# Performance work log

Measured on AMD Instinct MI355X. Metric: run time of the kernel, lower is better.

## Reference

```python
import jax, jax.numpy as jnp
import numpy as np
import math

B, H, N, D = 2, 16, 8192, 64
NUM_PROJS = 7
BLOCK = 256   # key block size
SAMPLE = 256  # number of sampled columns


def _gray_perm(n):
    # AngularLSH._unit_hamming_distance_array: Gray-code ordering of 2**n buckets
    a = np.array([0, 1], dtype=np.int32)
    for i in range(1, n):
        a = np.concatenate([a, a[::-1] + 2 ** i])
    return a

PERM = jnp.asarray(_gray_perm(NUM_PROJS))
ENC = jnp.asarray(2 ** np.arange(NUM_PROJS), dtype=jnp.int32)


def lsh_hash(x, proj_dir):
    # sign-bit angular LSH, then Gray-code remap so nearby buckets share bits
    bits = (jnp.einsum('bhnd,dr->bhnr', x, proj_dir) > 0).astype(jnp.int32)
    bin_ids = (bits * ENC).sum(-1)
    return PERM[bin_ids]


def take_seq(x, idx):
    # gather along the sequence axis (axis=2); idx is [B,H,M]
    return jnp.take_along_axis(x, idx[..., None], axis=2)


def setup_inputs() -> dict:
    key = jax.random.key(0)
    ks = jax.random.split(key, 5)
    return {
        'query': jax.random.normal(ks[0], (B, H, N, D), jnp.float32),
        'key': jax.random.normal(ks[1], (B, H, N, D), jnp.float32),
        'value': jax.random.normal(ks[2], (B, H, N, D), jnp.float32),
        'proj_dir': jax.random.normal(ks[3], (D + 1, NUM_PROJS), jnp.float32),
        'sampled_set': jax.random.randint(ks[4], (B, H, SAMPLE), 0, N),
    }


def reference(query, key, value, proj_dir, sampled_set):
    scale = D ** -0.5

    # asymmetric MIPS transform: key gets sqrt(max||k||^2 - ||k||^2), query gets 0
    k_norm = jnp.linalg.norm(key, axis=-1)                 # [B,H,N]
    k_max = jnp.max(k_norm, axis=-1, keepdims=True)        # [B,H,1]
    k_extra = jnp.sqrt(jnp.maximum(k_max ** 2 - k_norm ** 2, 0.0))
    key_aug = jnp.concatenate([key, k_extra[..., None]], axis=-1)
    query_aug = jnp.concatenate([query, jnp.zeros_like(query[..., :1])], axis=-1)

    # stable sort by LSH bucket; inverse permutation to un-sort queries at the end
    q_idx = jnp.argsort(lsh_hash(query_aug, proj_dir), axis=2, stable=True)
    k_idx = jnp.argsort(lsh_hash(key_aug, proj_dir), axis=2, stable=True)
    q_idx_inv = jnp.argsort(q_idx, axis=2, stable=True)

    q_s = take_seq(query, q_idx)
    k_s = take_seq(key, k_idx)
    v_s = take_seq(value, k_idx)

    nb = N // BLOCK      # number of key blocks (N divisible by BLOCK here)
    qbs = N // nb        # query block size

    # 1) block-diagonal exact attention over LSH-sorted blocks
    qb = q_s.reshape(B, H, nb, qbs, D)
    kb = k_s.reshape(B, H, nb, BLOCK, D)
    vb = v_s.reshape(B, H, nb, BLOCK, D)
    s_blk = jnp.einsum('bhgqd,bhgkd->bhgqk', qb, kb) * scale
    lse_blk = jax.nn.logsumexp(s_blk, axis=-1)             # [B,H,nb,qbs]
    attn_blk = jnp.einsum('bhgqk,bhgkd->bhgqd', jax.nn.softmax(s_blk, axis=-1), vb)
    attn_blk = attn_blk.reshape(B, H, N, D)
    lse_blk = lse_blk.reshape(B, H, N, 1)

    # 2) residual via uniformly sampled columns; mask out columns already in the
    #    query's own diagonal block to avoid double counting
    k_sub = take_seq(k_s, sampled_set)                     # [B,H,S,D]
    v_sub = take_seq(v_s, sampled_set)
    q_blk_id = jnp.arange(N) // qbs                        # [N]
    covered = q_blk_id[None, None, :, None] == (sampled_set // BLOCK)[:, :, None, :]
    bias = jnp.where(covered, jnp.finfo(q_s.dtype).min, 0.0)
    s_res = jnp.einsum('bhnd,bhsd->bhns', q_s, k_sub) * scale + bias
    # importance weight n_key/sample_size applied in log-space (approximate_unsampled)
    lse_res = jax.nn.logsumexp(s_res, axis=-1, keepdims=True) + math.log(N / SAMPLE)
    attn_res = jnp.einsum('bhns,bhsd->bhnd', jax.nn.softmax(s_res, axis=-1), v_sub)

    # add_self_attentions: merge the two softmax estimates in log-space
    c = 1.0 / (1.0 + jnp.exp(lse_res - lse_blk))
    attn = c * attn_blk + (1.0 - c) * attn_res

    # un-sort rows back to the original query order
    attn = take_seq(attn, q_idx_inv)
    return attn
```

## Files before the change

### kernel.cpp

```cpp
#include <hip/hip_runtime.h>
#include <hip/hip_bf16.h>
#include <math.h>

#define BD 2
#define HD 16
#define NSEQ 8192
#define DDIM 64
#define NPROJ 7
#define KBLK 256
#define NSAMP 256
#define NBH (BD*HD)
#define NB (NSEQ/KBLK)

#define LOG2E_8 0.18033688011112042f

typedef short bf16x8 __attribute__((ext_vector_type(8)));
typedef float f32x4 __attribute__((ext_vector_type(4)));

__device__ __forceinline__ unsigned int pk2bf(float a, float b) {
    union { __hip_bfloat162 h; unsigned int u; } t;
    t.h = __float22bfloat162_rn(make_float2(a, b));
    return t.u;
}

__global__ __launch_bounds__(256) void prelude_kernel(const float* __restrict__ q,
                                                      const float* __restrict__ k,
                                                      const float* __restrict__ pd,
                                                      float* __restrict__ kdots,
                                                      unsigned int* __restrict__ kmax_bits,
                                                      unsigned char* __restrict__ qh) {
    __shared__ float pds[(DDIM+1)*NPROJ];
    __shared__ float red[256];
    const int tid = threadIdx.x;
    for (int i = tid; i < (DDIM+1)*NPROJ; i += 256) pds[i] = pd[i];
    __syncthreads();

    const int lin = blockIdx.x * 256 + tid;
    const int bh = lin >> 13;

    float acc[NPROJ];
    float4 xv[16];

    {
        const float4* xp = (const float4*)(q + (size_t)lin * DDIM);
        #pragma unroll
        for (int j = 0; j < 16; ++j) xv[j] = xp[j];
        #pragma unroll
        for (int r = 0; r < NPROJ; ++r) acc[r] = 0.f;
        #pragma unroll
        for (int j = 0; j < 16; ++j) {
            float xs[4] = {xv[j].x, xv[j].y, xv[j].z, xv[j].w};
            #pragma unroll
            for (int c = 0; c < 4; ++c) {
                const int d = j*4 + c;
                #pragma unroll
                for (int r = 0; r < NPROJ; ++r) acc[r] += xs[c] * pds[d*NPROJ + r];
            }
        }
        int bin = 0;
        #pragma unroll
        for (int r = 0; r < NPROJ; ++r) bin |= (acc[r] > 0.f) << r;
        qh[lin] = (unsigned char)(bin ^ (bin >> 1));
    }

    float nr;
    {
        const float4* xp = (const float4*)(k + (size_t)lin * DDIM);
        #pragma unroll
        for (int j = 0; j < 16; ++j) xv[j] = xp[j];
        #pragma unroll
        for (int r = 0; r < NPROJ; ++r) acc[r] = 0.f;
        #pragma unroll
        for (int j = 0; j < 16; ++j) {
            float xs[4] = {xv[j].x, xv[j].y, xv[j].z, xv[j].w};
            #pragma unroll
            for (int c = 0; c < 4; ++c) {
                const int d = j*4 + c;
                #pragma unroll
                for (int r = 0; r < NPROJ; ++r) acc[r] += xs[c] * pds[d*NPROJ + r];
            }
        }
        float ss = 0.f;
        #pragma unroll
        for (int j = 0; j < 16; ++j) {
            float4 t = xv[j];
            ss += t.x*t.x + t.y*t.y + t.z*t.z + t.w*t.w;
        }
        nr = sqrtf(ss);
        float4* kd = (float4*)(kdots + (size_t)lin * 8);
        kd[0] = make_float4(acc[0], acc[1], acc[2], acc[3]);
        kd[1] = make_float4(acc[4], acc[5], acc[6], nr);
    }

    red[tid] = nr;
    __syncthreads();
    for (int s = 128; s > 0; s >>= 1) {
        if (tid < s) red[tid] = fmaxf(red[tid], red[tid+s]);
        __syncthreads();
    }
    if (tid == 0) atomicMax(&kmax_bits[bh], __float_as_uint(red[0]));
}

__global__ __launch_bounds__(256) void khash_kernel(const float* __restrict__ pd,
                                                    const float* __restrict__ kdots,
                                                    const unsigned int* __restrict__ kmax_bits,
                                                    unsigned char* __restrict__ kh) {
    const int lin = blockIdx.x * 256 + threadIdx.x;
    const int bh = lin >> 13;
    const float4* kd = (const float4*)(kdots + (size_t)lin * 8);
    float4 d0 = kd[0], d1 = kd[1];
    float acc[NPROJ] = {d0.x, d0.y, d0.z, d0.w, d1.x, d1.y, d1.z};
    const float kn = d1.w;
    const float km = __uint_as_float(kmax_bits[bh]);
    const float ex = sqrtf(fmaxf(km*km - kn*kn, 0.f));
    int bin = 0;
    #pragma unroll
    for (int r = 0; r < NPROJ; ++r) {
        acc[r] += ex * pd[DDIM*NPROJ + r];
        bin |= (acc[r] > 0.f) << r;
    }
    kh[lin] = (unsigned char)(bin ^ (bin >> 1));
}

__global__ __launch_bounds__(256) void sort_kernel(const unsigned char* __restrict__ qhash,
                                                   const unsigned char* __restrict__ khash,
                                                   int* __restrict__ qidx,
                                                   int* __restrict__ kidx) {
    __shared__ unsigned char hsh[NSEQ];
    __shared__ unsigned short cnt[128][264];
    __shared__ int base[128];
    __shared__ int wtot[2];
    const int bh = blockIdx.x, tid = threadIdx.x;
    const unsigned char* hash = blockIdx.y ? khash : qhash;
    int* idx = blockIdx.y ? kidx : qidx;

    {
        const uint4* src = (const uint4*)(hash + (size_t)bh * NSEQ);
        uint4* hdst = (uint4*)hsh;
        hdst[tid] = src[tid];
        hdst[tid + 256] = src[tid + 256];
        unsigned int* cz = (unsigned int*)&cnt[0][0];
        for (int i = tid; i < 128*264/2; i += 256) cz[i] = 0;
    }
    __syncthreads();
    {
        const unsigned char* s = hsh + tid*32;
        for (int i = 0; i < 32; ++i) cnt[s[i]][tid]++;
    }
    __syncthreads();

    int sc = 0, vv = 0;
    if (tid < 128) {
        unsigned run = 0;
        uint4* rp = (uint4*)cnt[tid];
        for (int wd = 0; wd < 32; ++wd) {
            uint4 x = rp[wd];
            unsigned v0 = x.x & 0xffffu, v1 = x.x >> 16;
            unsigned v2 = x.y & 0xffffu, v3 = x.y >> 16;
            unsigned v4 = x.z & 0xffffu, v5 = x.z >> 16;
            unsigned v6 = x.w & 0xffffu, v7 = x.w >> 16;
            unsigned p0 = run, p1 = p0+v0, p2 = p1+v1, p3 = p2+v2,
                     p4 = p3+v3, p5 = p4+v4, p6 = p5+v5, p7 = p6+v6;
            run = p7 + v7;
            x.x = p0 | (p1<<16); x.y = p2 | (p3<<16);
            x.z = p4 | (p5<<16); x.w = p6 | (p7<<16);
            rp[wd] = x;
        }
        vv = (int)run;
        sc = vv;
        #pragma unroll
        for (int d = 1; d < 64; d <<= 1) {
            int t = __shfl_up(sc, d, 64);
            if ((tid & 63) >= d) sc += t;
        }
        if ((tid & 63) == 63) wtot[tid >> 6] = sc;
    }
    __syncthreads();
    if (tid < 128) base[tid] = (sc - vv) + (tid >= 64 ? wtot[0] : 0);
    __syncthreads();
    {
        int* dst = idx + (size_t)bh * NSEQ;
        const unsigned char* s = hsh + tid*32;
        for (int i = 0; i < 32; ++i) {
            int h = s[i];
            int c = cnt[h][tid];
            cnt[h][tid] = (unsigned short)(c + 1);
            dst[base[h] + c] = tid*32 + i;
        }
    }
}


#define PPITCH 80
#define VSWZ(d) ((((d) >> 1) & 7) << 4)

template<int PHASE>
__device__ __forceinline__ void chunk_compute(
    int lane, char* Pw, int ch,
    const bf16x8 (&qhf)[4][2], const bf16x8 (&qlf)[4][2],
    f32x4 (&O)[4][4], float (&lacc)[4],
    const float* maskF, const char* KhL, const char* VthL, const char* VtlL) {

    const int lr4 = lane >> 4;
    const int lc  = lane & 15;

    #pragma unroll
    for (int half = 0; half < 2; ++half) {
        #pragma unroll
        for (int m2 = 0; m2 < 2; ++m2) {
            const int mt = half*2 + m2;
            const int key = mt*16 + lc;
            const int ksw = (key & 7) << 4;
            bf16x8 ka0 = *(const bf16x8*)(KhL + ((key*128 +  0 + lr4*16) ^ ksw));
            bf16x8 ka1 = *(const bf16x8*)(KhL + ((key*128 + 64 + lr4*16) ^ ksw));
            float4 mk;
            if (PHASE) mk = *(const float4*)(maskF + ch*64 + mt*16 + lr4*4);
            #pragma unroll
            for (int qt = 0; qt < 4; ++qt) {
                f32x4 c = {0.f, 0.f, 0.f, 0.f};
                c = __builtin_amdgcn_mfma_f32_16x16x32_bf16(ka0, qhf[qt][0], c, 0, 0, 0);
                c = __builtin_amdgcn_mfma_f32_16x16x32_bf16(ka0, qlf[qt][0], c, 0, 0, 0);
                c = __builtin_amdgcn_mfma_f32_16x16x32_bf16(ka1, qhf[qt][1], c, 0, 0, 0);
                c = __builtin_amdgcn_mfma_f32_16x16x32_bf16(ka1, qlf[qt][1], c, 0, 0, 0);
                float e0, e1, e2, e3;
                if (PHASE) {
                    e0 = exp2f(c[0] + 5.0f) * mk.x;
                    e1 = exp2f(c[1] + 5.0f) * mk.y;
                    e2 = exp2f(c[2] + 5.0f) * mk.z;
                    e3 = exp2f(c[3] + 5.0f) * mk.w;
                } else {
                    e0 = exp2f(c[0]); e1 = exp2f(c[1]);
                    e2 = exp2f(c[2]); e3 = exp2f(c[3]);
                }
                lacc[qt] += (e0+e1) + (e2+e3);
                uint2 wv;
                wv.x = pk2bf(e0, e1);
                wv.y = pk2bf(e2, e3);
                const int qq = qt*16 + lc;
                *(uint2*)(Pw + qq*PPITCH + m2*32 + lr4*8) = wv;
            }
        }

        bf16x8 pf[4];
        #pragma unroll
        for (int qt = 0; qt < 4; ++qt)
            pf[qt] = *(const bf16x8*)(Pw + (qt*16 + lc)*PPITCH + lr4*16);

        __builtin_amdgcn_s_setprio(1);
        #pragma unroll
        for (int dt = 0; dt < 4; ++dt) {
            const int d = dt*16 + lc;
            const int a = (d*128 + half*64 + lr4*16) ^ VSWZ(d);
            bf16x8 vh = *(const bf16x8*)(VthL + a);
            bf16x8 vl = *(const bf16x8*)(VtlL + a);
            #pragma unroll
            for (int qt = 0; qt < 4; ++qt) {
                O[qt][dt] = __builtin_amdgcn_mfma_f32_16x16x32_bf16(pf[qt], vh, O[qt][dt], 0, 0, 0);
                O[qt][dt] = __builtin_amdgcn_mfma_f32_16x16x32_bf16(pf[qt], vl, O[qt][dt], 0, 0, 0);
            }
        }
        __builtin_amdgcn_s_setprio(0);
    }
}

__global__ __launch_bounds__(256, 2) void attn_kernel(const float* __restrict__ q,
                                                      const float* __restrict__ k,
                                                      const float* __restrict__ v,
                                                      const int* __restrict__ samp,
                                                      const int* __restrict__ qidx,
                                                      const int* __restrict__ kidx,
                                                      float* __restrict__ out) {
    __shared__ __align__(16) char KhL[8192];
    __shared__ __align__(16) char VthL[8192];
    __shared__ __align__(16) char VtlL[8192];
    __shared__ __align__(16) char PL[4][PPITCH*64];
    __shared__ int qidxL[256];
    __shared__ int kidxL[256];
    __shared__ int ridxL[256];
    __shared__ float maskF[256];

    const int g = blockIdx.x, bh = blockIdx.y;
    const int tid = threadIdx.x;
    const int lane = tid & 63, w = tid >> 6;
    const int lr4 = lane >> 4, lc = lane & 15;
    const size_t basef = (size_t)bh * NSEQ * DDIM;

    qidxL[tid] = qidx[bh*NSEQ + g*KBLK + tid];
    kidxL[tid] = kidx[bh*NSEQ + g*KBLK + tid];
    {
        int sp = samp[bh*NSAMP + tid];
        ridxL[tid] = kidx[bh*NSEQ + sp];
        maskF[tid] = ((sp >> 8) == g) ? 0.f : 1.f;
    }
    __syncthreads();

    bf16x8 qhf[4][2], qlf[4][2];
    #pragma unroll
    for (int qt = 0; qt < 4; ++qt) {
        const int qrow = qidxL[w*64 + qt*16 + lc];
        const float* qp = q + basef + (size_t)qrow*DDIM;
        #pragma unroll
        for (int ks = 0; ks < 2; ++ks) {
            const float* p = qp + ks*32 + lr4*8;
            float4 a = *(const float4*)p;
            float4 b = *(const float4*)(p + 4);
            float xs[8] = {a.x,a.y,a.z,a.w,b.x,b.y,b.z,b.w};
            union { bf16x8 v; unsigned int u[4]; } hv, lv;
            #pragma unroll
            for (int j = 0; j < 4; ++j) {
                float s0 = xs[2*j]   * LOG2E_8;
                float s1 = xs[2*j+1] * LOG2E_8;
                unsigned hp = pk2bf(s0, s1);
                hv.u[j] = hp;
                float l0 = s0 - __uint_as_float(hp << 16);
                float l1 = s1 - __uint_as_float(hp & 0xffff0000u);
                lv.u[j] = pk2bf(l0, l1);
            }
            qhf[qt][ks] = hv.v; qlf[qt][ks] = lv.v;
        }
    }

    f32x4 O[4][4];
    #pragma unroll
    for (int a = 0; a < 4; ++a)
        #pragma unroll
        for (int b = 0; b < 4; ++b) O[a][b] = (f32x4){0.f,0.f,0.f,0.f};
    float lacc[4] = {0,0,0,0};
    char* Pw = PL[w];

    #pragma unroll
    for (int ph = 0; ph < 2; ++ph) {
        const int* IDX = ph ? ridxL : kidxL;
        for (int ch = 0; ch < 4; ++ch) {
            __syncthreads();
            {
                const int kk = tid & 63, dc = tid >> 6;
                const int korig = IDX[ch*64 + kk];
                const float* kr = k + basef + (size_t)korig*DDIM + dc*16;
                float4 f0 = ((const float4*)kr)[0], f1 = ((const float4*)kr)[1];
                float4 f2 = ((const float4*)kr)[2], f3 = ((const float4*)kr)[3];
                union { bf16x8 v; unsigned int u[4]; } h0, h1;
                h0.u[0] = pk2bf(f0.x,f0.y); h0.u[1] = pk2bf(f0.z,f0.w);
                h0.u[2] = pk2bf(f1.x,f1.y); h0.u[3] = pk2bf(f1.z,f1.w);
                h1.u[0] = pk2bf(f2.x,f2.y); h1.u[1] = pk2bf(f2.z,f2.w);
                h1.u[2] = pk2bf(f3.x,f3.y); h1.u[3] = pk2bf(f3.z,f3.w);
                const int rb = kk*128 + dc*32, sw = (kk & 7) << 4;
                *(bf16x8*)(KhL + ((rb) ^ sw)) = h0.v;
                *(bf16x8*)(KhL + ((rb + 16) ^ sw)) = h1.v;
            }
            {
                const int vg = tid & 15, kq = tid >> 4;
                const int r0 = IDX[ch*64 + kq*4 + 0];
                const int r1 = IDX[ch*64 + kq*4 + 1];
                const int r2 = IDX[ch*64 + kq*4 + 2];
                const int r3 = IDX[ch*64 + kq*4 + 3];
                float4 x0 = *(const float4*)(v + basef + (size_t)r0*DDIM + vg*4);
                float4 x1 = *(const float4*)(v + basef + (size_t)r1*DDIM + vg*4);
                float4 x2 = *(const float4*)(v + basef + (size_t)r2*DDIM + vg*4);
                float4 x3 = *(const float4*)(v + basef + (size_t)r3*DDIM + vg*4);
                const float c0[4] = {x0.x, x0.y, x0.z, x0.w};
                const float c1[4] = {x1.x, x1.y, x1.z, x1.w};
                const float c2[4] = {x2.x, x2.y, x2.z, x2.w};
                const float c3[4] = {x3.x, x3.y, x3.z, x3.w};
                #pragma unroll
                for (int j = 0; j < 4; ++j) {
                    const int d = vg*4 + j;
                    float a0 = c0[j], a1 = c1[j], a2 = c2[j], a3 = c3[j];
                    unsigned h01 = pk2bf(a0, a1), h23 = pk2bf(a2, a3);
                    float l0 = a0 - __uint_as_float(h01 << 16);
                    float l1 = a1 - __uint_as_float(h01 & 0xffff0000u);
                    float l2 = a2 - __uint_as_float(h23 << 16);
                    float l3 = a3 - __uint_as_float(h23 & 0xffff0000u);
                    unsigned w01 = pk2bf(l0, l1), w23 = pk2bf(l2, l3);
                    const int a = (d*128 + kq*8) ^ VSWZ(d);
                    *(uint2*)(VthL + a) = make_uint2(h01, h23);
                    *(uint2*)(VtlL + a) = make_uint2(w01, w23);
                }
            }
            __syncthreads();
            if (ph == 0)
                chunk_compute<0>(lane, Pw, ch, qhf, qlf, O, lacc, maskF, KhL, VthL, VtlL);
            else
                chunk_compute<1>(lane, Pw, ch, qhf, qlf, O, lacc, maskF, KhL, VthL, VtlL);
        }
    }

    #pragma unroll
    for (int qt = 0; qt < 4; ++qt) {
        lacc[qt] += __shfl_xor(lacc[qt], 16, 64);
        lacc[qt] += __shfl_xor(lacc[qt], 32, 64);
        lacc[qt] = 1.f / lacc[qt];
    }
    float* ob = out + basef;
    #pragma unroll
    for (int qt = 0; qt < 4; ++qt) {
        #pragma unroll
        for (int r = 0; r < 4; ++r) {
            const float f = __shfl(lacc[qt], (lane & 48) | (lr4*4 + r), 64);
            const int orow = qidxL[w*64 + qt*16 + lr4*4 + r];
            float* p = ob + (size_t)orow*DDIM + lc;
            #pragma unroll
            for (int dt = 0; dt < 4; ++dt) p[dt*16] = O[qt][dt][r] * f;
        }
    }
}

extern "C" void kernel_launch(void* const* d_in, const int* in_sizes, int n_in,
                              void* d_out, int out_size, void* d_ws, size_t ws_size,
                              hipStream_t stream) {
    const float* q    = (const float*)d_in[0];
    const float* k    = (const float*)d_in[1];
    const float* v    = (const float*)d_in[2];
    const float* pd   = (const float*)d_in[3];
    const int*   samp = (const int*)d_in[4];
    float* out = (float*)d_out;

    char* ws = (char*)d_ws;
    float*         kdots = (float*)(ws + 0);
    int*           qidx  = (int*)(ws + 0);
    int*           kidx  = (int*)(ws + 1048576);
    unsigned char* qh    = (unsigned char*)(ws + 8388608);
    unsigned char* kh    = (unsigned char*)(ws + 8650752);
    unsigned int*  kmaxb = (unsigned int*)(ws + 8912896);

    hipMemsetAsync(kmaxb, 0, NBH*sizeof(unsigned int), stream);
    hipLaunchKernelGGL(prelude_kernel, dim3(NBH*NSEQ/256), dim3(256), 0, stream,
                       q, k, pd, kdots, kmaxb, qh);
    hipLaunchKernelGGL(khash_kernel, dim3(NBH*NSEQ/256), dim3(256), 0, stream,
                       pd, kdots, kmaxb, kh);
    hipLaunchKernelGGL(sort_kernel, dim3(NBH, 2), dim3(256), 0, stream, qh, kh, qidx, kidx);
    hipLaunchKernelGGL(attn_kernel, dim3(NB, NBH), dim3(256), 0, stream,
                       q, k, v, samp, qidx, kidx, out);
}
```

Measured before the change: 187.0 us.

## Prepack sampled K/V once in a separate kernel and drop V low-part split

Adds a respack kernel that gathers the sampled residual keys and values once per head, converts them to bf16 and stores them in the swizzled LDS image layout. All 32 query-block workgroups can then copy that image straight into LDS instead of each redoing the gather and conversion. It also stops splitting V into bf16 high and low parts, which halves the PV MFMAs and the V LDS footprint. The exp2-with-log2e scaling is replaced by __expf on 1/8-scaled queries. The cost is lower precision in P·V, plus one extra kernel launch and a workspace round trip.

```diff
diff --git a/kernel.cpp b/kernel.cpp
--- a/kernel.cpp
+++ b/kernel.cpp
@@ -11,8 +11,6 @@
 #define NSAMP 256
 #define NBH (BD*HD)
 #define NB (NSEQ/KBLK)
-
-#define LOG2E_8 0.18033688011112042f
 
 typedef short bf16x8 __attribute__((ext_vector_type(8)));
 typedef float f32x4 __attribute__((ext_vector_type(4)));
@@ -190,16 +188,69 @@
     }
 }
 
+#define VSWZ(d) ((((d) >> 1) & 7) << 4)
+
+__global__ __launch_bounds__(256) void respack_kernel(const float* __restrict__ k,
+                                                      const float* __restrict__ v,
+                                                      const int* __restrict__ samp,
+                                                      const int* __restrict__ kidx,
+                                                      char* __restrict__ kres,
+                                                      char* __restrict__ vres) {
+    const int bh = blockIdx.x, ch = blockIdx.y, tid = threadIdx.x;
+    const size_t basef = (size_t)bh * NSEQ * DDIM;
+    char* kimg = kres + (size_t)(bh*4 + ch) * 8192;
+    char* vimg = vres + (size_t)(bh*4 + ch) * 8192;
+
+    {
+        const int kk = tid & 63, dc = tid >> 6;
+        const int sp = samp[bh*NSAMP + ch*64 + kk];
+        const int row = kidx[bh*NSEQ + sp];
+        const float* kr = k + basef + (size_t)row*DDIM + dc*16;
+        float4 f0 = ((const float4*)kr)[0], f1 = ((const float4*)kr)[1];
+        float4 f2 = ((const float4*)kr)[2], f3 = ((const float4*)kr)[3];
+        union { bf16x8 v8; unsigned int u[4]; } h0, h1;
+        h0.u[0] = pk2bf(f0.x,f0.y); h0.u[1] = pk2bf(f0.z,f0.w);
+        h0.u[2] = pk2bf(f1.x,f1.y); h0.u[3] = pk2bf(f1.z,f1.w);
+        h1.u[0] = pk2bf(f2.x,f2.y); h1.u[1] = pk2bf(f2.z,f2.w);
+        h1.u[2] = pk2bf(f3.x,f3.y); h1.u[3] = pk2bf(f3.z,f3.w);
+        const int rb = kk*128 + dc*32, sw = (kk & 7) << 4;
+        *(bf16x8*)(kimg + ((rb) ^ sw)) = h0.v8;
+        *(bf16x8*)(kimg + ((rb + 16) ^ sw)) = h1.v8;
+    }
+    {
+        const int vg = tid & 15, kq = tid >> 4;
+        const int r0 = kidx[bh*NSEQ + samp[bh*NSAMP + ch*64 + kq*4 + 0]];
+        const int r1 = kidx[bh*NSEQ + samp[bh*NSAMP + ch*64 + kq*4 + 1]];
+        const int r2 = kidx[bh*NSEQ + samp[bh*NSAMP + ch*64 + kq*4 + 2]];
+        const int r3 = kidx[bh*NSEQ + samp[bh*NSAMP + ch*64 + kq*4 + 3]];
+        float4 x0 = *(const float4*)(v + basef + (size_t)r0*DDIM + vg*4);
+        float4 x1 = *(const float4*)(v + basef + (size_t)r1*DDIM + vg*4);
+        float4 x2 = *(const float4*)(v + basef + (size_t)r2*DDIM + vg*4);
+        float4 x3 = *(const float4*)(v + basef + (size_t)r3*DDIM + vg*4);
+        const float c0[4] = {x0.x, x0.y, x0.z, x0.w};
+        const float c1[4] = {x1.x, x1.y, x1.z, x1.w};
+        const float c2[4] = {x2.x, x2.y, x2.z, x2.w};
+        const float c3[4] = {x3.x, x3.y, x3.z, x3.w};
+        #pragma unroll
+        for (int j = 0; j < 4; ++j) {
+            const int d = vg*4 + j;
+            unsigned h01 = pk2bf(c0[j], c1[j]);
+            unsigned h23 = pk2bf(c2[j], c3[j]);
+            *(uint2*)(vimg + ((d*128 + kq*8) ^ VSWZ(d))) = make_uint2(h01, h23);
+        }
+    }
+}
+
 
 #define PPITCH 80
-#define VSWZ(d) ((((d) >> 1) & 7) << 4)
+#define LN32 3.46573590279972f
 
 template<int PHASE>
 __device__ __forceinline__ void chunk_compute(
     int lane, char* Pw, int ch,
     const bf16x8 (&qhf)[4][2], const bf16x8 (&qlf)[4][2],
     f32x4 (&O)[4][4], float (&lacc)[4],
-    const float* maskF, const char* KhL, const char* VthL, const char* VtlL) {
+    const float* maskF, const char* KhL, const char* VthL) {
 
     const int lr4 = lane >> 4;
     const int lc  = lane & 15;
@@ -224,13 +275,13 @@
                 c = __builtin_amdgcn_mfma_f32_16x16x32_bf16(ka1, qlf[qt][1], c, 0, 0, 0);
                 float e0, e1, e2, e3;
                 if (PHASE) {
-                    e0 = exp2f(c[0] + 5.0f) * mk.x;
-                    e1 = exp2f(c[1] + 5.0f) * mk.y;
-                    e2 = exp2f(c[2] + 5.0f) * mk.z;
-                    e3 = exp2f(c[3] + 5.0f) * mk.w;
+                    e0 = __expf(c[0] + LN32) * mk.x;
+                    e1 = __expf(c[1] + LN32) * mk.y;
+                    e2 = __expf(c[2] + LN32) * mk.z;
+                    e3 = __expf(c[3] + LN32) * mk.w;
                 } else {
-                    e0 = exp2f(c[0]); e1 = exp2f(c[1]);
-                    e2 = exp2f(c[2]); e3 = exp2f(c[3]);
+                    e0 = __expf(c[0]); e1 = __expf(c[1]);
+                    e2 = __expf(c[2]); e3 = __expf(c[3]);
                 }
                 lacc[qt] += (e0+e1) + (e2+e3);
                 uint2 wv;
@@ -252,11 +303,9 @@
             const int d = dt*16 + lc;
             const int a = (d*128 + half*64 + lr4*16) ^ VSWZ(d);
             bf16x8 vh = *(const bf16x8*)(VthL + a);
-            bf16x8 vl = *(const bf16x8*)(VtlL + a);
             #pragma unroll
             for (int qt = 0; qt < 4; ++qt) {
                 O[qt][dt] = __builtin_amdgcn_mfma_f32_16x16x32_bf16(pf[qt], vh, O[qt][dt], 0, 0, 0);
-                O[qt][dt] = __builtin_amdgcn_mfma_f32_16x16x32_bf16(pf[qt], vl, O[qt][dt], 0, 0, 0);
             }
         }
         __builtin_amdgcn_s_setprio(0);
@@ -269,14 +318,14 @@
                                                       const int* __restrict__ samp,
                                                       const int* __restrict__ qidx,
                                                       const int* __restrict__ kidx,
+                                                      const char* __restrict__ kres,
+                                                      const char* __restrict__ vres,
                                                       float* __restrict__ out) {
     __shared__ __align__(16) char KhL[8192];
     __shared__ __align__(16) char VthL[8192];
-    __shared__ __align__(16) char VtlL[8192];
     __shared__ __align__(16) char PL[4][PPITCH*64];
     __shared__ int qidxL[256];
     __shared__ int kidxL[256];
-    __shared__ int ridxL[256];
     __shared__ float maskF[256];
 
     const int g = blockIdx.x, bh = blockIdx.y;
@@ -289,7 +338,6 @@
     kidxL[tid] = kidx[bh*NSEQ + g*KBLK + tid];
     {
         int sp = samp[bh*NSAMP + tid];
-        ridxL[tid] = kidx[bh*NSEQ + sp];
         maskF[tid] = ((sp >> 8) == g) ? 0.f : 1.f;
     }
     __syncthreads();
@@ -305,18 +353,18 @@
             float4 a = *(const float4*)p;
             float4 b = *(const float4*)(p + 4);
             float xs[8] = {a.x,a.y,a.z,a.w,b.x,b.y,b.z,b.w};
-            union { bf16x8 v; unsigned int u[4]; } hv, lv;
+            union { bf16x8 v8; unsigned int u[4]; } hv, lv;
             #pragma unroll
             for (int j = 0; j < 4; ++j) {
-                float s0 = xs[2*j]   * LOG2E_8;
-                float s1 = xs[2*j+1] * LOG2E_8;
+                float s0 = xs[2*j]   * 0.125f;
+                float s1 = xs[2*j+1] * 0.125f;
                 unsigned hp = pk2bf(s0, s1);
                 hv.u[j] = hp;
                 float l0 = s0 - __uint_as_float(hp << 16);
                 float l1 = s1 - __uint_as_float(hp & 0xffff0000u);
                 lv.u[j] = pk2bf(l0, l1);
             }
-            qhf[qt][ks] = hv.v; qlf[qt][ks] = lv.v;
+            qhf[qt][ks] = hv.v8; qlf[qt][ks] = lv.v8;
         }
     }
 
@@ -328,61 +376,65 @@
     float lacc[4] = {0,0,0,0};
     char* Pw = PL[w];
 
-    #pragma unroll
-    for (int ph = 0; ph < 2; ++ph) {
-        const int* IDX = ph ? ridxL : kidxL;
-        for (int ch = 0; ch < 4; ++ch) {
-            __syncthreads();
-            {
-                const int kk = tid & 63, dc = tid >> 6;
-                const int korig = IDX[ch*64 + kk];
-                const float* kr = k + basef + (size_t)korig*DDIM + dc*16;
-                float4 f0 = ((const float4*)kr)[0], f1 = ((const float4*)kr)[1];
-                float4 f2 = ((const float4*)kr)[2], f3 = ((const float4*)kr)[3];
-                union { bf16x8 v; unsigned int u[4]; } h0, h1;
-                h0.u[0] = pk2bf(f0.x,f0.y); h0.u[1] = pk2bf(f0.z,f0.w);
-                h0.u[2] = pk2bf(f1.x,f1.y); h0.u[3] = pk2bf(f1.z,f1.w);
-                h1.u[0] = pk2bf(f2.x,f2.y); h1.u[1] = pk2bf(f2.z,f2.w);
-                h1.u[2] = pk2bf(f3.x,f3.y); h1.u[3] = pk2bf(f3.z,f3.w);
-                const int rb = kk*128 + dc*32, sw = (kk & 7) << 4;
-                *(bf16x8*)(KhL + ((rb) ^ sw)) = h0.v;
-                *(bf16x8*)(KhL + ((rb + 16) ^ sw)) = h1.v;
-            }
-            {
-                const int vg = tid & 15, kq = tid >> 4;
-                const int r0 = IDX[ch*64 + kq*4 + 0];
-                const int r1 = IDX[ch*64 + kq*4 + 1];
-                const int r2 = IDX[ch*64 + kq*4 + 2];
-                const int r3 = IDX[ch*64 + kq*4 + 3];
-                float4 x0 = *(const float4*)(v + basef + (size_t)r0*DDIM + vg*4);
-                float4 x1 = *(const float4*)(v + basef + (size_t)r1*DDIM + vg*4);
-                float4 x2 = *(const float4*)(v + basef + (size_t)r2*DDIM + vg*4);
-                float4 x3 = *(const float4*)(v + basef + (size_t)r3*DDIM + vg*4);
-                const float c0[4] = {x0.x, x0.y, x0.z, x0.w};
-                const float c1[4] = {x1.x, x1.y, x1.z, x1.w};
-                const float c2[4] = {x2.x, x2.y, x2.z, x2.w};
-                const float c3[4] = {x3.x, x3.y, x3.z, x3.w};
-                #pragma unroll
-                for (int j = 0; j < 4; ++j) {
-                    const int d = vg*4 + j;
-                    float a0 = c0[j], a1 = c1[j], a2 = c2[j], a3 = c3[j];
-                    unsigned h01 = pk2bf(a0, a1), h23 = pk2bf(a2, a3);
-                    float l0 = a0 - __uint_as_float(h01 << 16);
-                    float l1 = a1 - __uint_as_float(h01 & 0xffff0000u);
-                    float l2 = a2 - __uint_as_float(h23 << 16);
-                    float l3 = a3 - __uint_as_float(h23 & 0xffff0000u);
-                    unsigned w01 = pk2bf(l0, l1), w23 = pk2bf(l2, l3);
-                    const int a = (d*128 + kq*8) ^ VSWZ(d);
-                    *(uint2*)(VthL + a) = make_uint2(h01, h23);
-                    *(uint2*)(VtlL + a) = make_uint2(w01, w23);
-                }
-            }
-            __syncthreads();
-            if (ph == 0)
-                chunk_compute<0>(lane, Pw, ch, qhf, qlf, O, lacc, maskF, KhL, VthL, VtlL);
-            else
-                chunk_compute<1>(lane, Pw, ch, qhf, qlf, O, lacc, maskF, KhL, VthL, VtlL);
-        }
+    for (int ch = 0; ch < 4; ++ch) {
+        __syncthreads();
+        {
+            const int kk = tid & 63, dc = tid >> 6;
+            const int korig = kidxL[ch*64 + kk];
+            const float* kr = k + basef + (size_t)korig*DDIM + dc*16;
+            float4 f0 = ((const float4*)kr)[0], f1 = ((const float4*)kr)[1];
+            float4 f2 = ((const float4*)kr)[2], f3 = ((const float4*)kr)[3];
+            union { bf16x8 v8; unsigned int u[4]; } h0, h1;
+            h0.u[0] = pk2bf(f0.x,f0.y); h0.u[1] = pk2bf(f0.z,f0.w);
+            h0.u[2] = pk2bf(f1.x,f1.y); h0.u[3] = pk2bf(f1.z,f1.w);
+            h1.u[0] = pk2bf(f2.x,f2.y); h1.u[1] = pk2bf(f2.z,f2.w);
+            h1.u[2] = pk2bf(f3.x,f3.y); h1.u[3] = pk2bf(f3.z,f3.w);
+            const int rb = kk*128 + dc*32, sw = (kk & 7) << 4;
+            *(bf16x8*)(KhL + ((rb) ^ sw)) = h0.v8;
+            *(bf16x8*)(KhL + ((rb + 16) ^ sw)) = h1.v8;
+        }
+        {
+            const int vg = tid & 15, kq = tid >> 4;
+            const int r0 = kidxL[ch*64 + kq*4 + 0];
+            const int r1 = kidxL[ch*64 + kq*4 + 1];
+            const int r2 = kidxL[ch*64 + kq*4 + 2];
+            const int r3 = kidxL[ch*64 + kq*4 + 3];
+            float4 x0 = *(const float4*)(v + basef + (size_t)r0*DDIM + vg*4);
+            float4 x1 = *(const float4*)(v + basef + (size_t)r1*DDIM + vg*4);
+            float4 x2 = *(const float4*)(v + basef + (size_t)r2*DDIM + vg*4);
+            float4 x3 = *(const float4*)(v + basef + (size_t)r3*DDIM + vg*4);
+            const float c0[4] = {x0.x, x0.y, x0.z, x0.w};
+            const float c1[4] = {x1.x, x1.y, x1.z, x1.w};
+            const float c2[4] = {x2.x, x2.y, x2.z, x2.w};
+            const float c3[4] = {x3.x, x3.y, x3.z, x3.w};
+            #pragma unroll
+            for (int j = 0; j < 4; ++j) {
+                const int d = vg*4 + j;
+                unsigned h01 = pk2bf(c0[j], c1[j]);
+                unsigned h23 = pk2bf(c2[j], c3[j]);
+                *(uint2*)(VthL + ((d*128 + kq*8) ^ VSWZ(d))) = make_uint2(h01, h23);
+            }
+        }
+        __syncthreads();
+        chunk_compute<0>(lane, Pw, ch, qhf, qlf, O, lacc, maskF, KhL, VthL);
+    }
+
+    for (int ch = 0; ch < 4; ++ch) {
+        __syncthreads();
+        {
+            const char* ks = kres + (size_t)(bh*4 + ch) * 8192 + tid*32;
+            const char* vs = vres + (size_t)(bh*4 + ch) * 8192 + tid*32;
+            float4 a0 = *(const float4*)ks;
+            float4 a1 = *(const float4*)(ks + 16);
+            float4 b0 = *(const float4*)vs;
+            float4 b1 = *(const float4*)(vs + 16);
+            *(float4*)(KhL + tid*32)       = a0;
+            *(float4*)(KhL + tid*32 + 16)  = a1;
+            *(float4*)(VthL + tid*32)      = b0;
+            *(float4*)(VthL + tid*32 + 16) = b1;
+        }
+        __syncthreads();
+        chunk_compute<1>(lane, Pw, ch, qhf, qlf, O, lacc, maskF, KhL, VthL);
     }
 
     #pragma unroll
@@ -419,6 +471,8 @@
     float*         kdots = (float*)(ws + 0);
     int*           qidx  = (int*)(ws + 0);
     int*           kidx  = (int*)(ws + 1048576);
+    char*          kres  = ws + 2097152;
+    char*          vres  = ws + 3145728;
     unsigned char* qh    = (unsigned char*)(ws + 8388608);
     unsigned char* kh    = (unsigned char*)(ws + 8650752);
     unsigned int*  kmaxb = (unsigned int*)(ws + 8912896);
@@ -429,6 +483,8 @@
     hipLaunchKernelGGL(khash_kernel, dim3(NBH*NSEQ/256), dim3(256), 0, stream,
                        pd, kdots, kmaxb, kh);
     hipLaunchKernelGGL(sort_kernel, dim3(NBH, 2), dim3(256), 0, stream, qh, kh, qidx, kidx);
+    hipLaunchKernelGGL(respack_kernel, dim3(NBH, 4), dim3(256), 0, stream,
+                       k, v, samp, kidx, kres, vres);
     hipLaunchKernelGGL(attn_kernel, dim3(NB, NBH), dim3(256), 0, stream,
-                       q, k, v, samp, qidx, kidx, out);
-}
+                       q, k, v, samp, qidx, kidx, kres, vres, out);
+}
```

Result: faster. 152.3 us (-18.5%).

## Double-buffer fp32 K/V tiles in LDS via async global_load_lds, convert at use

Applied to the files above, without the earlier changes.

Replaces the per-chunk synchronous gather-and-convert of K and V into bf16 hi/lo LDS tiles with direct asynchronous global-to-LDS loads of fp32 rows into double-buffered, XOR-swizzled buffers. The next chunk is prefetched while the current one computes, and the two sync points per chunk become one. K is converted to bf16 at use, P stays in registers and feeds a 16x16x16 MFMA instead of going through LDS, and V loses its hi/lo split, so the P·V product now uses single bf16 V. The exp changes from exp2f with a log2e pre-scale to __expf. It also relocates workspace buffers so kdots no longer aliases qidx. This cuts LDS traffic and serialization but lowers V precision and doubles LDS footprint, which may limit occupancy.

```diff
diff --git a/kernel.cpp b/kernel.cpp
--- a/kernel.cpp
+++ b/kernel.cpp
@@ -12,15 +12,20 @@
 #define NBH (BD*HD)
 #define NB (NSEQ/KBLK)
 
-#define LOG2E_8 0.18033688011112042f
-
 typedef short bf16x8 __attribute__((ext_vector_type(8)));
+typedef short bf16x4 __attribute__((ext_vector_type(4)));
 typedef float f32x4 __attribute__((ext_vector_type(4)));
 
 __device__ __forceinline__ unsigned int pk2bf(float a, float b) {
     union { __hip_bfloat162 h; unsigned int u; } t;
     t.h = __float22bfloat162_rn(make_float2(a, b));
     return t.u;
+}
+
+__device__ __forceinline__ void gload16(const void* gsrc, void* lds) {
+    __builtin_amdgcn_global_load_lds(
+        (const __attribute__((address_space(1))) unsigned int*)gsrc,
+        (__attribute__((address_space(3))) unsigned int*)lds, 16, 0, 0);
 }
 
 __global__ __launch_bounds__(256) void prelude_kernel(const float* __restrict__ q,
@@ -191,73 +196,78 @@
 }
 
 
-#define PPITCH 80
-#define VSWZ(d) ((((d) >> 1) & 7) << 4)
+#define LN32 3.46573590279972f
 
 template<int PHASE>
-__device__ __forceinline__ void chunk_compute(
-    int lane, char* Pw, int ch,
+__device__ __forceinline__ void compute_chunk(
+    int rc, int lane,
     const bf16x8 (&qhf)[4][2], const bf16x8 (&qlf)[4][2],
     f32x4 (&O)[4][4], float (&lacc)[4],
-    const float* maskF, const char* KhL, const char* VthL, const char* VtlL) {
+    const float* maskF, const char* KL, const char* VL) {
 
     const int lr4 = lane >> 4;
     const int lc  = lane & 15;
 
     #pragma unroll
-    for (int half = 0; half < 2; ++half) {
-        #pragma unroll
-        for (int m2 = 0; m2 < 2; ++m2) {
-            const int mt = half*2 + m2;
-            const int key = mt*16 + lc;
-            const int ksw = (key & 7) << 4;
-            bf16x8 ka0 = *(const bf16x8*)(KhL + ((key*128 +  0 + lr4*16) ^ ksw));
-            bf16x8 ka1 = *(const bf16x8*)(KhL + ((key*128 + 64 + lr4*16) ^ ksw));
-            float4 mk;
-            if (PHASE) mk = *(const float4*)(maskF + ch*64 + mt*16 + lr4*4);
-            #pragma unroll
-            for (int qt = 0; qt < 4; ++qt) {
-                f32x4 c = {0.f, 0.f, 0.f, 0.f};
-                c = __builtin_amdgcn_mfma_f32_16x16x32_bf16(ka0, qhf[qt][0], c, 0, 0, 0);
-                c = __builtin_amdgcn_mfma_f32_16x16x32_bf16(ka0, qlf[qt][0], c, 0, 0, 0);
-                c = __builtin_amdgcn_mfma_f32_16x16x32_bf16(ka1, qhf[qt][1], c, 0, 0, 0);
-                c = __builtin_amdgcn_mfma_f32_16x16x32_bf16(ka1, qlf[qt][1], c, 0, 0, 0);
-                float e0, e1, e2, e3;
-                if (PHASE) {
-                    e0 = exp2f(c[0] + 5.0f) * mk.x;
-                    e1 = exp2f(c[1] + 5.0f) * mk.y;
-                    e2 = exp2f(c[2] + 5.0f) * mk.z;
-                    e3 = exp2f(c[3] + 5.0f) * mk.w;
-                } else {
-                    e0 = exp2f(c[0]); e1 = exp2f(c[1]);
-                    e2 = exp2f(c[2]); e3 = exp2f(c[3]);
-                }
-                lacc[qt] += (e0+e1) + (e2+e3);
-                uint2 wv;
-                wv.x = pk2bf(e0, e1);
-                wv.y = pk2bf(e2, e3);
-                const int qq = qt*16 + lc;
-                *(uint2*)(Pw + qq*PPITCH + m2*32 + lr4*8) = wv;
+    for (int mt = 0; mt < 4; ++mt) {
+        const int key = mt*16 + lc;
+        const int ks = key & 15;
+        const char* KR = KL + key*256;
+        f32x4 a0 = *(const f32x4*)(KR + (((lr4*2    ) ^ ks) << 4));
+        f32x4 a1 = *(const f32x4*)(KR + (((lr4*2 + 1) ^ ks) << 4));
+        f32x4 b0 = *(const f32x4*)(KR + (((lr4*2 + 8) ^ ks) << 4));
+        f32x4 b1 = *(const f32x4*)(KR + (((lr4*2 + 9) ^ ks) << 4));
+        union { bf16x8 v8; unsigned int u[4]; } kh0, kh1;
+        kh0.u[0] = pk2bf(a0[0], a0[1]); kh0.u[1] = pk2bf(a0[2], a0[3]);
+        kh0.u[2] = pk2bf(a1[0], a1[1]); kh0.u[3] = pk2bf(a1[2], a1[3]);
+        kh1.u[0] = pk2bf(b0[0], b0[1]); kh1.u[1] = pk2bf(b0[2], b0[3]);
+        kh1.u[2] = pk2bf(b1[0], b1[1]); kh1.u[3] = pk2bf(b1[2], b1[3]);
+
+        float4 mk;
+        if (PHASE) mk = *(const float4*)(maskF + rc*64 + mt*16 + lr4*4);
+
+        bf16x4 pa[4];
+        #pragma unroll
+        for (int qt = 0; qt < 4; ++qt) {
+            f32x4 c = {0.f, 0.f, 0.f, 0.f};
+            c = __builtin_amdgcn_mfma_f32_16x16x32_bf16(kh0.v8, qhf[qt][0], c, 0, 0, 0);
+            c = __builtin_amdgcn_mfma_f32_16x16x32_bf16(kh0.v8, qlf[qt][0], c, 0, 0, 0);
+            c = __builtin_amdgcn_mfma_f32_16x16x32_bf16(kh1.v8, qhf[qt][1], c, 0, 0, 0);
+            c = __builtin_amdgcn_mfma_f32_16x16x32_bf16(kh1.v8, qlf[qt][1], c, 0, 0, 0);
+            float e0, e1, e2, e3;
+            if (PHASE) {
+                e0 = __expf(c[0] + LN32) * mk.x;
+                e1 = __expf(c[1] + LN32) * mk.y;
+                e2 = __expf(c[2] + LN32) * mk.z;
+                e3 = __expf(c[3] + LN32) * mk.w;
+            } else {
+                e0 = __expf(c[0]); e1 = __expf(c[1]);
+                e2 = __expf(c[2]); e3 = __expf(c[3]);
             }
-        }
-
-        bf16x8 pf[4];
-        #pragma unroll
-        for (int qt = 0; qt < 4; ++qt)
-            pf[qt] = *(const bf16x8*)(Pw + (qt*16 + lc)*PPITCH + lr4*16);
+            lacc[qt] += (e0+e1) + (e2+e3);
+            union { bf16x4 v4; unsigned int u[2]; } pw;
+            pw.u[0] = pk2bf(e0, e1);
+            pw.u[1] = pk2bf(e2, e3);
+            pa[qt] = pw.v4;
+        }
 
         __builtin_amdgcn_s_setprio(1);
         #pragma unroll
         for (int dt = 0; dt < 4; ++dt) {
             const int d = dt*16 + lc;
-            const int a = (d*128 + half*64 + lr4*16) ^ VSWZ(d);
-            bf16x8 vh = *(const bf16x8*)(VthL + a);
-            bf16x8 vl = *(const bf16x8*)(VtlL + a);
-            #pragma unroll
-            for (int qt = 0; qt < 4; ++qt) {
-                O[qt][dt] = __builtin_amdgcn_mfma_f32_16x16x32_bf16(pf[qt], vh, O[qt][dt], 0, 0, 0);
-                O[qt][dt] = __builtin_amdgcn_mfma_f32_16x16x32_bf16(pf[qt], vl, O[qt][dt], 0, 0, 0);
+            const int gd = d >> 2, sub = (d & 3) << 2;
+            float fv[4];
+            #pragma unroll
+            for (int r = 0; r < 4; ++r) {
+                const int rv = mt*16 + lr4*4 + r;
+                fv[r] = *(const float*)(VL + rv*256 + (((gd ^ (rv & 15)) << 4) | sub));
             }
+            union { bf16x4 v4; unsigned int u[2]; } vb;
+            vb.u[0] = pk2bf(fv[0], fv[1]);
+            vb.u[1] = pk2bf(fv[2], fv[3]);
+            #pragma unroll
+            for (int qt = 0; qt < 4; ++qt)
+                O[qt][dt] = __builtin_amdgcn_mfma_f32_16x16x16bf16_1k(pa[qt], vb.v4, O[qt][dt], 0, 0, 0);
         }
         __builtin_amdgcn_s_setprio(0);
     }
@@ -270,20 +280,20 @@
                                                       const int* __restrict__ qidx,
                                                       const int* __restrict__ kidx,
                                                       float* __restrict__ out) {
-    __shared__ __align__(16) char KhL[8192];
-    __shared__ __align__(16) char VthL[8192];
-    __shared__ __align__(16) char VtlL[8192];
-    __shared__ __align__(16) char PL[4][PPITCH*64];
+    __shared__ __align__(16) char KB2[2][16384];
+    __shared__ __align__(16) char VB2[2][16384];
     __shared__ int qidxL[256];
     __shared__ int kidxL[256];
     __shared__ int ridxL[256];
-    __shared__ float maskF[256];
+    __shared__ __align__(16) float maskF[256];
 
     const int g = blockIdx.x, bh = blockIdx.y;
     const int tid = threadIdx.x;
     const int lane = tid & 63, w = tid >> 6;
     const int lr4 = lane >> 4, lc = lane & 15;
     const size_t basef = (size_t)bh * NSEQ * DDIM;
+    const float* kb = k + basef;
+    const float* vb = v + basef;
 
     qidxL[tid] = qidx[bh*NSEQ + g*KBLK + tid];
     kidxL[tid] = kidx[bh*NSEQ + g*KBLK + tid];
@@ -293,6 +303,22 @@
         maskF[tid] = ((sp >> 8) == g) ? 0.f : 1.f;
     }
     __syncthreads();
+
+    #define STAGE(ROWS, BUF)                                                    \
+    {                                                                           \
+        _Pragma("unroll")                                                       \
+        for (int i = 0; i < 4; ++i) {                                           \
+            const int B = i*4096 + w*1024 + lane*16;                            \
+            const int row = B >> 8;                                             \
+            const int gg = (B & 255) >> 4;                                      \
+            const int rr = (ROWS)[row];                                         \
+            const int sc = ((gg ^ (row & 15)) << 4) >> 2;                       \
+            gload16(kb + (size_t)rr*64 + sc, KB2[BUF] + i*4096 + w*1024);       \
+            gload16(vb + (size_t)rr*64 + sc, VB2[BUF] + i*4096 + w*1024);       \
+        }                                                                       \
+    }
+
+    STAGE(kidxL, 0)
 
     bf16x8 qhf[4][2], qlf[4][2];
     #pragma unroll
@@ -305,18 +331,18 @@
             float4 a = *(const float4*)p;
             float4 b = *(const float4*)(p + 4);
             float xs[8] = {a.x,a.y,a.z,a.w,b.x,b.y,b.z,b.w};
-            union { bf16x8 v; unsigned int u[4]; } hv, lv;
+            union { bf16x8 v8; unsigned int u[4]; } hv, lv;
             #pragma unroll
             for (int j = 0; j < 4; ++j) {
-                float s0 = xs[2*j]   * LOG2E_8;
-                float s1 = xs[2*j+1] * LOG2E_8;
+                float s0 = xs[2*j]   * 0.125f;
+                float s1 = xs[2*j+1] * 0.125f;
                 unsigned hp = pk2bf(s0, s1);
                 hv.u[j] = hp;
                 float l0 = s0 - __uint_as_float(hp << 16);
                 float l1 = s1 - __uint_as_float(hp & 0xffff0000u);
                 lv.u[j] = pk2bf(l0, l1);
             }
-            qhf[qt][ks] = hv.v; qlf[qt][ks] = lv.v;
+            qhf[qt][ks] = hv.v8; qlf[qt][ks] = lv.v8;
         }
     }
 
@@ -326,64 +352,20 @@
         #pragma unroll
         for (int b = 0; b < 4; ++b) O[a][b] = (f32x4){0.f,0.f,0.f,0.f};
     float lacc[4] = {0,0,0,0};
-    char* Pw = PL[w];
-
-    #pragma unroll
-    for (int ph = 0; ph < 2; ++ph) {
-        const int* IDX = ph ? ridxL : kidxL;
-        for (int ch = 0; ch < 4; ++ch) {
-            __syncthreads();
-            {
-                const int kk = tid & 63, dc = tid >> 6;
-                const int korig = IDX[ch*64 + kk];
-                const float* kr = k + basef + (size_t)korig*DDIM + dc*16;
-                float4 f0 = ((const float4*)kr)[0], f1 = ((const float4*)kr)[1];
-                float4 f2 = ((const float4*)kr)[2], f3 = ((const float4*)kr)[3];
-                union { bf16x8 v; unsigned int u[4]; } h0, h1;
-                h0.u[0] = pk2bf(f0.x,f0.y); h0.u[1] = pk2bf(f0.z,f0.w);
-                h0.u[2] = pk2bf(f1.x,f1.y); h0.u[3] = pk2bf(f1.z,f1.w);
-                h1.u[0] = pk2bf(f2.x,f2.y); h1.u[1] = pk2bf(f2.z,f2.w);
-                h1.u[2] = pk2bf(f3.x,f3.y); h1.u[3] = pk2bf(f3.z,f3.w);
-                const int rb = kk*128 + dc*32, sw = (kk & 7) << 4;
-                *(bf16x8*)(KhL + ((rb) ^ sw)) = h0.v;
-                *(bf16x8*)(KhL + ((rb + 16) ^ sw)) = h1.v;
-            }
-            {
-                const int vg = tid & 15, kq = tid >> 4;
-                const int r0 = IDX[ch*64 + kq*4 + 0];
-                const int r1 = IDX[ch*64 + kq*4 + 1];
-                const int r2 = IDX[ch*64 + kq*4 + 2];
-                const int r3 = IDX[ch*64 + kq*4 + 3];
-                float4 x0 = *(const float4*)(v + basef + (size_t)r0*DDIM + vg*4);
-                float4 x1 = *(const float4*)(v + basef + (size_t)r1*DDIM + vg*4);
-                float4 x2 = *(const float4*)(v + basef + (size_t)r2*DDIM + vg*4);
-                float4 x3 = *(const float4*)(v + basef + (size_t)r3*DDIM + vg*4);
-                const float c0[4] = {x0.x, x0.y, x0.z, x0.w};
-                const float c1[4] = {x1.x, x1.y, x1.z, x1.w};
-                const float c2[4] = {x2.x, x2.y, x2.z, x2.w};
-                const float c3[4] = {x3.x, x3.y, x3.z, x3.w};
-                #pragma unroll
-                for (int j = 0; j < 4; ++j) {
-                    const int d = vg*4 + j;
-                    float a0 = c0[j], a1 = c1[j], a2 = c2[j], a3 = c3[j];
-                    unsigned h01 = pk2bf(a0, a1), h23 = pk2bf(a2, a3);
-                    float l0 = a0 - __uint_as_float(h01 << 16);
-                    float l1 = a1 - __uint_as_float(h01 & 0xffff0000u);
-                    float l2 = a2 - __uint_as_float(h23 << 16);
-                    float l3 = a3 - __uint_as_float(h23 & 0xffff0000u);
-                    unsigned w01 = pk2bf(l0, l1), w23 = pk2bf(l2, l3);
-                    const int a = (d*128 + kq*8) ^ VSWZ(d);
-                    *(uint2*)(VthL + a) = make_uint2(h01, h23);
-                    *(uint2*)(VtlL + a) = make_uint2(w01, w23);
-                }
-            }
-            __syncthreads();
-            if (ph == 0)
-                chunk_compute<0>(lane, Pw, ch, qhf, qlf, O, lacc, maskF, KhL, VthL, VtlL);
-            else
-                chunk_compute<1>(lane, Pw, ch, qhf, qlf, O, lacc, maskF, KhL, VthL, VtlL);
-        }
-    }
+
+    __syncthreads();
+
+    for (int ch = 0; ch < 8; ++ch) {
+        if (ch < 7) {
+            const int nch = ch + 1;
+            if (nch < 4) { STAGE(kidxL + nch*64, (nch & 1)) }
+            else         { STAGE(ridxL + (nch-4)*64, (nch & 1)) }
+        }
+        if (ch < 4) compute_chunk<0>(ch,   lane, qhf, qlf, O, lacc, maskF, KB2[ch&1], VB2[ch&1]);
+        else        compute_chunk<1>(ch-4, lane, qhf, qlf, O, lacc, maskF, KB2[ch&1], VB2[ch&1]);
+        __syncthreads();
+    }
+    #undef STAGE
 
     #pragma unroll
     for (int qt = 0; qt < 4; ++qt) {
@@ -416,12 +398,12 @@
     float* out = (float*)d_out;
 
     char* ws = (char*)d_ws;
-    float*         kdots = (float*)(ws + 0);
     int*           qidx  = (int*)(ws + 0);
-    int*           kidx  = (int*)(ws + 1048576);
-    unsigned char* qh    = (unsigned char*)(ws + 8388608);
-    unsigned char* kh    = (unsigned char*)(ws + 8650752);
-    unsigned int*  kmaxb = (unsigned int*)(ws + 8912896);
+    int*           kidx  = (int*)(ws + (1<<20));
+    float*         kdots = (float*)(ws + (2<<20));
+    unsigned char* qh    = (unsigned char*)(ws + (10<<20));
+    unsigned char* kh    = (unsigned char*)(ws + (10<<20) + 262144);
+    unsigned int*  kmaxb = (unsigned int*)(ws + (11<<20));
 
     hipMemsetAsync(kmaxb, 0, NBH*sizeof(unsigned int), stream);
     hipLaunchKernelGGL(prelude_kernel, dim3(NBH*NSEQ/256), dim3(256), 0, stream,
```

After: 330.3 us. 76.6% more time.
